# Kernel optimization log

Measured on AMD Instinct MI355X. Metric: run time of the kernel, lower is better.

The kernel has to match this reference:

```python
import jax, jax.numpy as jnp
import numpy as np

BASE = 10000.0

def positional_encoding(seq_len, dim, dtype=jnp.float32):
    # standard sinusoidal PE: pe[p, 2i] = sin(p / BASE^(2i/dim)), pe[p, 2i+1] = cos(...)
    pos = jnp.arange(seq_len, dtype=dtype)[:, None]            # [S,1]
    idx = jnp.arange(0, dim, 2, dtype=dtype)[None, :]          # [1,dim/2]
    ang = pos / jnp.power(BASE, idx / dim)                     # [S,dim/2]
    pe = jnp.zeros((seq_len, dim), dtype=dtype)
    pe = pe.at[:, 0::2].set(jnp.sin(ang)).at[:, 1::2].set(jnp.cos(ang))
    return pe

def setup_inputs() -> dict:
    key = jax.random.key(0)
    ks = jax.random.split(key, 5)
    B, S, H, D = 16, 2048, 128, 64
    x = jax.random.normal(ks[0], (B, S, H), dtype=jnp.float32)
    Wq = jax.random.normal(ks[1], (H, D), dtype=jnp.float32) * (H ** -0.5)
    Wk = jax.random.normal(ks[2], (H, D), dtype=jnp.float32) * (H ** -0.5)
    Wv = jax.random.normal(ks[3], (H, D), dtype=jnp.float32) * (H ** -0.5)
    Wf = jax.random.normal(ks[4], (D, 1), dtype=jnp.float32) * (D ** -0.5)
    bf = jnp.zeros((1,), dtype=jnp.float32)
    return {"x": x, "Wq": Wq, "Wk": Wk, "Wv": Wv, "Wf": Wf, "bf": bf}

def reference(x, Wq, Wk, Wv, Wf, bf):
    B, S, H = x.shape
    xp = x + positional_encoding(S, H, x.dtype)[None]          # add PE, broadcast over batch
    Q = jnp.einsum('bsh,hd->bsd', xp, Wq)
    K = jnp.einsum('bsh,hd->bsd', xp, Wk)
    V = jnp.einsum('bsh,hd->bsd', xp, Wv)
    D = K.shape[-1]
    scores = jnp.einsum('bqd,bkd->bqk', Q, K) / jnp.sqrt(jnp.asarray(D, x.dtype))
    # NOTE: softmax over dim=1 (the QUERY axis), per the original nn.Softmax(dim=1)
    attn = jax.nn.softmax(scores, axis=1)                      # [B,S,S]
    z = jnp.einsum('bqk,bkd->bqd', attn, V)                    # [B,S,D]
    out = (jnp.einsum('bsd,do->bso', z, Wf) + bf).squeeze(-1)  # [B,S]
    return out
```

## Files before the change

kernel.cpp:

```cpp
#include <hip/hip_runtime.h>
#include <math.h>

#define BATCH 16
#define SEQ   2048
#define HID   128
#define DIM   64

typedef __attribute__((ext_vector_type(8))) short bf16x8;
typedef __attribute__((ext_vector_type(4))) float f32x4;

#define QSCALE 0.18033688011112042f
#define C0_PE  0.07195578314043169f

static __device__ __forceinline__ ushort f2bf(float f) {
    union { float f; unsigned u; } v; v.f = f;
    unsigned r = v.u + 0x7FFFu + ((v.u >> 16) & 1u);
    return (ushort)(r >> 16);
}

static __device__ __forceinline__ float fast_exp2(float x) {
#if __has_builtin(__builtin_amdgcn_exp2f)
    return __builtin_amdgcn_exp2f(x);
#else
    return exp2f(x);
#endif
}

__global__ void k_prep(const float* __restrict__ Wq, const float* __restrict__ Wk,
                       const float* __restrict__ Wv, const float* __restrict__ Wf,
                       ushort* __restrict__ Wt, float* __restrict__ wvf) {
    const int tid = threadIdx.x;
    if (tid < HID) {
        float s = 0.f;
        #pragma unroll 8
        for (int d = 0; d < DIM; ++d) s += Wv[tid * DIM + d] * Wf[d];
        wvf[tid] = s;
    }
    for (int i = tid; i < 128 * 128; i += 256) {
        int col = i >> 7, k = i & 127;
        float v = (col < 64) ? Wq[k * DIM + col] * QSCALE : Wk[k * DIM + (col - 64)];
        Wt[i] = f2bf(v);
    }
}

__global__ __launch_bounds__(256) void k_qkv(
    const float* __restrict__ x, const ushort* __restrict__ Wt,
    const float* __restrict__ wvf, ushort* __restrict__ Qb,
    ushort* __restrict__ Kb, float* __restrict__ vf)
{
    const int tid  = threadIdx.x;
    const int wave = tid >> 6;
    const int lane = tid & 63;
    const int quad = lane >> 4;
    const int col  = lane & 15;
    const int rowbase = blockIdx.x * 64 + wave * 16;
    const int grow = rowbase + col;
    const float pos = (float)(grow & (SEQ - 1));

    bf16x8 af[4];
    float vpart = 0.f;
    #pragma unroll
    for (int c = 0; c < 4; ++c) {
        const float* xp = x + (size_t)grow * HID + quad * 8 + c * 32;
        float4 v0 = *(const float4*)(xp);
        float4 v1 = *(const float4*)(xp + 4);
        float t[8] = {v0.x, v0.y, v0.z, v0.w, v1.x, v1.y, v1.z, v1.w};
        #pragma unroll
        for (int jp = 0; jp < 4; ++jp) {
            int h = quad * 8 + c * 32 + jp * 2;
            float ang = pos * __expf(-(float)h * C0_PE);
            t[jp * 2]     += __sinf(ang);
            t[jp * 2 + 1] += __cosf(ang);
        }
        const float* wp = wvf + quad * 8 + c * 32;
        float4 w0 = *(const float4*)(wp);
        float4 w1 = *(const float4*)(wp + 4);
        vpart += t[0] * w0.x + t[1] * w0.y + t[2] * w0.z + t[3] * w0.w +
                 t[4] * w1.x + t[5] * w1.y + t[6] * w1.z + t[7] * w1.w;
        short* ap = (short*)&af[c];
        #pragma unroll
        for (int j = 0; j < 8; ++j) ap[j] = (short)f2bf(t[j]);
    }

    vpart += __shfl_xor(vpart, 16);
    vpart += __shfl_xor(vpart, 32);
    if (quad == 0) vf[grow] = vpart;

    #pragma unroll
    for (int t = 0; t < 8; ++t) {
        const ushort* wrow = Wt + (size_t)(t * 16 + col) * 128 + quad * 8;
        f32x4 acc = {0.f, 0.f, 0.f, 0.f};
        #pragma unroll
        for (int c = 0; c < 4; ++c) {
            bf16x8 bfr = *(const bf16x8*)(wrow + c * 32);
            acc = __builtin_amdgcn_mfma_f32_16x16x32_bf16(af[c], bfr, acc, 0, 0, 0);
        }
        const int cb = (t & 3) * 16 + col;
        ushort* dst = (t < 4) ? Qb : Kb;
        const int r0 = rowbase + quad * 4;
        #pragma unroll
        for (int r = 0; r < 4; ++r)
            dst[(size_t)(r0 + r) * DIM + cb] = f2bf(acc[r]);
    }
}

__global__ __launch_bounds__(512) void k_stats(
    const ushort* __restrict__ Qb, const ushort* __restrict__ Kb,
    const float* __restrict__ vf, float* __restrict__ wb)
{
    const int b    = blockIdx.y;
    const int k0   = blockIdx.x * 64;
    const int tid  = threadIdx.x;
    const int wave = tid >> 6;
    const int lane = tid & 63;
    const int quad = lane >> 4;
    const int col  = lane & 15;

    __shared__ float sl[8][64];

    bf16x8 kf[4][2];
    {
        const ushort* Kbase = Kb + ((size_t)(b * SEQ + k0)) * DIM;
        #pragma unroll
        for (int t = 0; t < 4; ++t)
            #pragma unroll
            for (int c = 0; c < 2; ++c)
                kf[t][c] = *(const bf16x8*)(Kbase + (size_t)(t * 16 + col) * DIM + quad * 8 + c * 32);
    }

    float l[4] = {0.f, 0.f, 0.f, 0.f};
    const ushort* Qrow = Qb + ((size_t)(b * SEQ + wave * 256 + col)) * DIM + quad * 8;

    for (int qi = 0; qi < 16; ++qi) {
        bf16x8 a0 = *(const bf16x8*)(Qrow);
        bf16x8 a1 = *(const bf16x8*)(Qrow + 32);
        Qrow += 16 * DIM;
        #pragma unroll
        for (int t = 0; t < 4; ++t) {
            f32x4 acc = {0.f, 0.f, 0.f, 0.f};
            acc = __builtin_amdgcn_mfma_f32_16x16x32_bf16(a0, kf[t][0], acc, 0, 0, 0);
            acc = __builtin_amdgcn_mfma_f32_16x16x32_bf16(a1, kf[t][1], acc, 0, 0, 0);
            l[t] += fast_exp2(acc.x) + fast_exp2(acc.y) +
                    fast_exp2(acc.z) + fast_exp2(acc.w);
        }
    }

    #pragma unroll
    for (int t = 0; t < 4; ++t) {
        l[t] += __shfl_xor(l[t], 16);
        l[t] += __shfl_xor(l[t], 32);
    }
    if (quad == 0) {
        #pragma unroll
        for (int t = 0; t < 4; ++t) sl[wave][t * 16 + col] = l[t];
    }
    __syncthreads();

    if (tid < 64) {
        float ll = 0.f;
        #pragma unroll
        for (int w = 0; w < 8; ++w) ll += sl[w][tid];
        size_t g = (size_t)b * SEQ + k0 + tid;
        wb[g] = vf[g] / ll;
    }
}

__global__ __launch_bounds__(512) void k_out(
    const ushort* __restrict__ Qb, const ushort* __restrict__ Kb,
    const float* __restrict__ wb, const float* __restrict__ bfp,
    float* __restrict__ outp)
{
    const int b    = blockIdx.y;
    const int q0   = blockIdx.x * 64;
    const int tid  = threadIdx.x;
    const int wave = tid >> 6;
    const int lane = tid & 63;
    const int quad = lane >> 4;
    const int col  = lane & 15;

    __shared__ float sred[8][64];

    bf16x8 qf[4][2];
    {
        const ushort* Qbase = Qb + ((size_t)(b * SEQ + q0)) * DIM;
        #pragma unroll
        for (int t = 0; t < 4; ++t)
            #pragma unroll
            for (int c = 0; c < 2; ++c)
                qf[t][c] = *(const bf16x8*)(Qbase + (size_t)(t * 16 + col) * DIM + quad * 8 + c * 32);
    }

    float rs[4][4] = {};
    const ushort* Krow = Kb + ((size_t)(b * SEQ + wave * 256 + col)) * DIM + quad * 8;
    const float*  wptr = wb + (size_t)b * SEQ + wave * 256 + col;

    for (int ki = 0; ki < 16; ++ki) {
        bf16x8 b0 = *(const bf16x8*)(Krow);
        bf16x8 b1 = *(const bf16x8*)(Krow + 32);
        Krow += 16 * DIM;
        float wc = *wptr; wptr += 16;
        #pragma unroll
        for (int t = 0; t < 4; ++t) {
            f32x4 acc = {0.f, 0.f, 0.f, 0.f};
            acc = __builtin_amdgcn_mfma_f32_16x16x32_bf16(qf[t][0], b0, acc, 0, 0, 0);
            acc = __builtin_amdgcn_mfma_f32_16x16x32_bf16(qf[t][1], b1, acc, 0, 0, 0);
            #pragma unroll
            for (int r = 0; r < 4; ++r)
                rs[t][r] += fast_exp2(acc[r]) * wc;
        }
    }

    #pragma unroll
    for (int t = 0; t < 4; ++t)
        #pragma unroll
        for (int r = 0; r < 4; ++r) {
            float v = rs[t][r];
            v += __shfl_xor(v, 1); v += __shfl_xor(v, 2);
            v += __shfl_xor(v, 4); v += __shfl_xor(v, 8);
            rs[t][r] = v;
        }

    if (col == 0) {
        #pragma unroll
        for (int t = 0; t < 4; ++t)
            #pragma unroll
            for (int r = 0; r < 4; ++r)
                sred[wave][t * 16 + quad * 4 + r] = rs[t][r];
    }
    __syncthreads();

    if (tid < 64) {
        float s = bfp[0];
        #pragma unroll
        for (int w = 0; w < 8; ++w) s += sred[w][tid];
        outp[(size_t)b * SEQ + q0 + tid] = s;
    }
}

extern "C" void kernel_launch(void* const* d_in, const int* in_sizes, int n_in,
                              void* d_out, int out_size, void* d_ws, size_t ws_size,
                              hipStream_t stream) {
    (void)in_sizes; (void)n_in; (void)out_size; (void)ws_size;
    const float* x  = (const float*)d_in[0];
    const float* Wq = (const float*)d_in[1];
    const float* Wk = (const float*)d_in[2];
    const float* Wv = (const float*)d_in[3];
    const float* Wf = (const float*)d_in[4];
    const float* bf = (const float*)d_in[5];
    float* outp = (float*)d_out;

    float*  wvf = (float*)d_ws;
    float*  vf  = wvf + 256;
    float*  wb  = vf + (size_t)BATCH * SEQ;
    ushort* Wt  = (ushort*)(wb + (size_t)BATCH * SEQ);
    ushort* Qb  = Wt + 128 * 128;
    ushort* Kb  = Qb + (size_t)BATCH * SEQ * DIM;

    k_prep<<<1, 256, 0, stream>>>(Wq, Wk, Wv, Wf, Wt, wvf);
    k_qkv<<<BATCH * SEQ / 64, 256, 0, stream>>>(x, Wt, wvf, Qb, Kb, vf);
    k_stats<<<dim3(SEQ / 64, BATCH), 512, 0, stream>>>(Qb, Kb, vf, wb);
    k_out<<<dim3(SEQ / 64, BATCH), 512, 0, stream>>>(Qb, Kb, wb, bf, outp);
}
```

Baseline: 139.2 us.

## Precompute PE table, split QKV waves by Q/K half, unroll attention loops by two

Adds a kernel that builds the sinusoidal positional-encoding table once, so the projection kernel loads it instead of recomputing sin/cos/exp for every batch row. The projection kernel now runs 512 threads, with each pair of waves sharing a row tile and one wave computing Q and the other K. It also uses packed bf16 conversion. The stats and output kernels process two 16-row K/Q tiles per iteration, which gives more independent MFMA chains and loads in flight. In exchange there is an extra launch and a 1MB table read, and register pressure rises in the unrolled loops.

```diff
diff --git a/kernel.cpp b/kernel.cpp
--- a/kernel.cpp
+++ b/kernel.cpp
@@ -1,4 +1,5 @@
 #include <hip/hip_runtime.h>
+#include <hip/hip_bf16.h>
 #include <math.h>
 
 #define BATCH 16
@@ -16,6 +17,12 @@
     union { float f; unsigned u; } v; v.f = f;
     unsigned r = v.u + 0x7FFFu + ((v.u >> 16) & 1u);
     return (ushort)(r >> 16);
+}
+
+static __device__ __forceinline__ ushort2 pk_bf16(float a, float b) {
+    union { __hip_bfloat162 h; ushort2 u; } v;
+    v.h = __float22bfloat162_rn(make_float2(a, b));
+    return v.u;
 }
 
 static __device__ __forceinline__ float fast_exp2(float x) {
@@ -24,6 +31,14 @@
 #else
     return exp2f(x);
 #endif
+}
+
+__global__ __launch_bounds__(256) void k_pe(float* __restrict__ pet) {
+    int i = blockIdx.x * 256 + threadIdx.x;
+    int pos = i >> 6, hp = i & 63;
+    float ang = (float)pos * __expf(-(float)(2 * hp) * C0_PE);
+    pet[pos * HID + 2 * hp]     = __sinf(ang);
+    pet[pos * HID + 2 * hp + 1] = __cosf(ang);
 }
 
 __global__ void k_prep(const float* __restrict__ Wq, const float* __restrict__ Wk,
@@ -43,60 +58,63 @@
     }
 }
 
-__global__ __launch_bounds__(256) void k_qkv(
-    const float* __restrict__ x, const ushort* __restrict__ Wt,
-    const float* __restrict__ wvf, ushort* __restrict__ Qb,
-    ushort* __restrict__ Kb, float* __restrict__ vf)
+__global__ __launch_bounds__(512) void k_qkv(
+    const float* __restrict__ x, const float* __restrict__ pet,
+    const ushort* __restrict__ Wt, const float* __restrict__ wvf,
+    ushort* __restrict__ Qb, ushort* __restrict__ Kb, float* __restrict__ vf)
 {
     const int tid  = threadIdx.x;
     const int wave = tid >> 6;
     const int lane = tid & 63;
     const int quad = lane >> 4;
     const int col  = lane & 15;
-    const int rowbase = blockIdx.x * 64 + wave * 16;
+    const int rowtile  = blockIdx.x * 4 + (wave >> 1);
+    const int colhalf  = wave & 1;
+    const int rowbase  = rowtile * 16;
     const int grow = rowbase + col;
-    const float pos = (float)(grow & (SEQ - 1));
+    const int pos  = grow & (SEQ - 1);
 
     bf16x8 af[4];
     float vpart = 0.f;
     #pragma unroll
     for (int c = 0; c < 4; ++c) {
-        const float* xp = x + (size_t)grow * HID + quad * 8 + c * 32;
+        const float* xp = x   + (size_t)grow * HID + quad * 8 + c * 32;
+        const float* pp = pet + (size_t)pos  * HID + quad * 8 + c * 32;
         float4 v0 = *(const float4*)(xp);
         float4 v1 = *(const float4*)(xp + 4);
-        float t[8] = {v0.x, v0.y, v0.z, v0.w, v1.x, v1.y, v1.z, v1.w};
-        #pragma unroll
-        for (int jp = 0; jp < 4; ++jp) {
-            int h = quad * 8 + c * 32 + jp * 2;
-            float ang = pos * __expf(-(float)h * C0_PE);
-            t[jp * 2]     += __sinf(ang);
-            t[jp * 2 + 1] += __cosf(ang);
-        }
-        const float* wp = wvf + quad * 8 + c * 32;
-        float4 w0 = *(const float4*)(wp);
-        float4 w1 = *(const float4*)(wp + 4);
-        vpart += t[0] * w0.x + t[1] * w0.y + t[2] * w0.z + t[3] * w0.w +
-                 t[4] * w1.x + t[5] * w1.y + t[6] * w1.z + t[7] * w1.w;
-        short* ap = (short*)&af[c];
-        #pragma unroll
-        for (int j = 0; j < 8; ++j) ap[j] = (short)f2bf(t[j]);
-    }
-
-    vpart += __shfl_xor(vpart, 16);
-    vpart += __shfl_xor(vpart, 32);
-    if (quad == 0) vf[grow] = vpart;
-
-    #pragma unroll
-    for (int t = 0; t < 8; ++t) {
-        const ushort* wrow = Wt + (size_t)(t * 16 + col) * 128 + quad * 8;
+        float4 p0 = *(const float4*)(pp);
+        float4 p1 = *(const float4*)(pp + 4);
+        float t[8] = {v0.x + p0.x, v0.y + p0.y, v0.z + p0.z, v0.w + p0.w,
+                      v1.x + p1.x, v1.y + p1.y, v1.z + p1.z, v1.w + p1.w};
+        if (colhalf == 0) {
+            const float* wp = wvf + quad * 8 + c * 32;
+            float4 w0 = *(const float4*)(wp);
+            float4 w1 = *(const float4*)(wp + 4);
+            vpart += t[0] * w0.x + t[1] * w0.y + t[2] * w0.z + t[3] * w0.w +
+                     t[4] * w1.x + t[5] * w1.y + t[6] * w1.z + t[7] * w1.w;
+        }
+        ushort2* ap = (ushort2*)&af[c];
+        #pragma unroll
+        for (int j = 0; j < 4; ++j) ap[j] = pk_bf16(t[2 * j], t[2 * j + 1]);
+    }
+
+    if (colhalf == 0) {
+        vpart += __shfl_xor(vpart, 16);
+        vpart += __shfl_xor(vpart, 32);
+        if (quad == 0) vf[grow] = vpart;
+    }
+
+    ushort* dst = colhalf ? Kb : Qb;
+    #pragma unroll
+    for (int t = 0; t < 4; ++t) {
+        const ushort* wrow = Wt + (size_t)((colhalf * 4 + t) * 16 + col) * 128 + quad * 8;
         f32x4 acc = {0.f, 0.f, 0.f, 0.f};
         #pragma unroll
         for (int c = 0; c < 4; ++c) {
             bf16x8 bfr = *(const bf16x8*)(wrow + c * 32);
             acc = __builtin_amdgcn_mfma_f32_16x16x32_bf16(af[c], bfr, acc, 0, 0, 0);
         }
-        const int cb = (t & 3) * 16 + col;
-        ushort* dst = (t < 4) ? Qb : Kb;
+        const int cb = t * 16 + col;
         const int r0 = rowbase + quad * 4;
         #pragma unroll
         for (int r = 0; r < 4; ++r)
@@ -131,17 +149,24 @@
     float l[4] = {0.f, 0.f, 0.f, 0.f};
     const ushort* Qrow = Qb + ((size_t)(b * SEQ + wave * 256 + col)) * DIM + quad * 8;
 
-    for (int qi = 0; qi < 16; ++qi) {
-        bf16x8 a0 = *(const bf16x8*)(Qrow);
-        bf16x8 a1 = *(const bf16x8*)(Qrow + 32);
-        Qrow += 16 * DIM;
+    for (int qi = 0; qi < 8; ++qi) {
+        bf16x8 a00 = *(const bf16x8*)(Qrow);
+        bf16x8 a01 = *(const bf16x8*)(Qrow + 32);
+        bf16x8 a10 = *(const bf16x8*)(Qrow + 16 * DIM);
+        bf16x8 a11 = *(const bf16x8*)(Qrow + 16 * DIM + 32);
+        Qrow += 32 * DIM;
         #pragma unroll
         for (int t = 0; t < 4; ++t) {
-            f32x4 acc = {0.f, 0.f, 0.f, 0.f};
-            acc = __builtin_amdgcn_mfma_f32_16x16x32_bf16(a0, kf[t][0], acc, 0, 0, 0);
-            acc = __builtin_amdgcn_mfma_f32_16x16x32_bf16(a1, kf[t][1], acc, 0, 0, 0);
-            l[t] += fast_exp2(acc.x) + fast_exp2(acc.y) +
-                    fast_exp2(acc.z) + fast_exp2(acc.w);
+            f32x4 acc0 = {0.f, 0.f, 0.f, 0.f};
+            f32x4 acc1 = {0.f, 0.f, 0.f, 0.f};
+            acc0 = __builtin_amdgcn_mfma_f32_16x16x32_bf16(a00, kf[t][0], acc0, 0, 0, 0);
+            acc0 = __builtin_amdgcn_mfma_f32_16x16x32_bf16(a01, kf[t][1], acc0, 0, 0, 0);
+            acc1 = __builtin_amdgcn_mfma_f32_16x16x32_bf16(a10, kf[t][0], acc1, 0, 0, 0);
+            acc1 = __builtin_amdgcn_mfma_f32_16x16x32_bf16(a11, kf[t][1], acc1, 0, 0, 0);
+            l[t] += fast_exp2(acc0.x) + fast_exp2(acc0.y) +
+                    fast_exp2(acc0.z) + fast_exp2(acc0.w) +
+                    fast_exp2(acc1.x) + fast_exp2(acc1.y) +
+                    fast_exp2(acc1.z) + fast_exp2(acc1.w);
         }
     }
 
@@ -194,19 +219,26 @@
     const ushort* Krow = Kb + ((size_t)(b * SEQ + wave * 256 + col)) * DIM + quad * 8;
     const float*  wptr = wb + (size_t)b * SEQ + wave * 256 + col;
 
-    for (int ki = 0; ki < 16; ++ki) {
-        bf16x8 b0 = *(const bf16x8*)(Krow);
-        bf16x8 b1 = *(const bf16x8*)(Krow + 32);
-        Krow += 16 * DIM;
-        float wc = *wptr; wptr += 16;
+    for (int ki = 0; ki < 8; ++ki) {
+        bf16x8 b00 = *(const bf16x8*)(Krow);
+        bf16x8 b01 = *(const bf16x8*)(Krow + 32);
+        bf16x8 b10 = *(const bf16x8*)(Krow + 16 * DIM);
+        bf16x8 b11 = *(const bf16x8*)(Krow + 16 * DIM + 32);
+        Krow += 32 * DIM;
+        float wc0 = wptr[0];
+        float wc1 = wptr[16];
+        wptr += 32;
         #pragma unroll
         for (int t = 0; t < 4; ++t) {
-            f32x4 acc = {0.f, 0.f, 0.f, 0.f};
-            acc = __builtin_amdgcn_mfma_f32_16x16x32_bf16(qf[t][0], b0, acc, 0, 0, 0);
-            acc = __builtin_amdgcn_mfma_f32_16x16x32_bf16(qf[t][1], b1, acc, 0, 0, 0);
+            f32x4 acc0 = {0.f, 0.f, 0.f, 0.f};
+            f32x4 acc1 = {0.f, 0.f, 0.f, 0.f};
+            acc0 = __builtin_amdgcn_mfma_f32_16x16x32_bf16(qf[t][0], b00, acc0, 0, 0, 0);
+            acc0 = __builtin_amdgcn_mfma_f32_16x16x32_bf16(qf[t][1], b01, acc0, 0, 0, 0);
+            acc1 = __builtin_amdgcn_mfma_f32_16x16x32_bf16(qf[t][0], b10, acc1, 0, 0, 0);
+            acc1 = __builtin_amdgcn_mfma_f32_16x16x32_bf16(qf[t][1], b11, acc1, 0, 0, 0);
             #pragma unroll
             for (int r = 0; r < 4; ++r)
-                rs[t][r] += fast_exp2(acc[r]) * wc;
+                rs[t][r] += fast_exp2(acc0[r]) * wc0 + fast_exp2(acc1[r]) * wc1;
         }
     }
 
@@ -252,12 +284,14 @@
     float*  wvf = (float*)d_ws;
     float*  vf  = wvf + 256;
     float*  wb  = vf + (size_t)BATCH * SEQ;
-    ushort* Wt  = (ushort*)(wb + (size_t)BATCH * SEQ);
+    float*  pet = wb + (size_t)BATCH * SEQ;
+    ushort* Wt  = (ushort*)(pet + (size_t)SEQ * HID);
     ushort* Qb  = Wt + 128 * 128;
     ushort* Kb  = Qb + (size_t)BATCH * SEQ * DIM;
 
+    k_pe<<<SEQ * (HID / 2) / 256, 256, 0, stream>>>(pet);
     k_prep<<<1, 256, 0, stream>>>(Wq, Wk, Wv, Wf, Wt, wvf);
-    k_qkv<<<BATCH * SEQ / 64, 256, 0, stream>>>(x, Wt, wvf, Qb, Kb, vf);
+    k_qkv<<<BATCH * SEQ / 64, 512, 0, stream>>>(x, pet, Wt, wvf, Qb, Kb, vf);
     k_stats<<<dim3(SEQ / 64, BATCH), 512, 0, stream>>>(Qb, Kb, vf, wb);
     k_out<<<dim3(SEQ / 64, BATCH), 512, 0, stream>>>(Qb, Kb, wb, bf, outp);
 }
```

Result: slower. 152.4 us (+9.5%).
